# Optimization experiments

Hardware: AMD Instinct MI355X
Metric: run time of the kernel (lower is better)

## Reference

```python
import jax, jax.numpy as jnp
import numpy as np

N_NODES = 10000
N_EDGES = 640000
D_IN = 128
D_OUT = 128


def setup_inputs() -> dict:
    key = jax.random.key(0)
    k_x, k_val, k_w, k_row, k_col = jax.random.split(key, 5)
    # Glorot init for weight, zeros for bias (matches _weight_init)
    limit = float(np.sqrt(6.0 / (D_IN + D_OUT)))
    weight = jax.random.uniform(k_w, (D_IN, D_OUT), jnp.float32, -limit, limit)
    return {
        "x": jax.random.normal(k_x, (N_NODES, D_IN), jnp.float32),
        "adj_val": jax.random.uniform(k_val, (N_EDGES,), jnp.float32),  # normalized edge weights of sparse adj
        "weight": weight,
        "bias": jnp.zeros((D_OUT,), jnp.float32),
        "adj_row": jax.random.randint(k_row, (N_EDGES,), 0, N_NODES, jnp.int32),
        "adj_col": jax.random.randint(k_col, (N_EDGES,), 0, N_NODES, jnp.int32),
    }


def reference(x, adj_val, weight, bias, adj_row, adj_col):
    # dense GEMM: h = x @ W  -> [N, D_OUT]
    h = jnp.matmul(x, weight)
    # SpMM with COO adjacency: out[r] = sum_{e: row[e]=r} val[e] * h[col[e]]
    msg = adj_val[:, None] * h[adj_col]  # [E, D_OUT] gather + scale
    out = jax.ops.segment_sum(msg, adj_row, num_segments=x.shape[0])
    return out + bias
```

## Files before the change

kernel.cpp:

```cpp
#include <hip/hip_runtime.h>

#define N_NODES 10000
#define N_EDGES 640000
#define D 128
#define NQ (N_EDGES / 4)

#define NCHUNK 128
#define QPC (NQ / NCHUNK)
#define GEMM_BLOCKS 157
#define GRID1 (NCHUNK + GEMM_BLOCKS)
#define NBUCK 625
#define CCAP 24
#define BSLOTS (NCHUNK * CCAP)
#define SPILLCAP 5000
#define CAP2 128
#define QPAD2 144
#define LSTR 136

typedef unsigned int uint32;
typedef unsigned short u16;
using short8 = __attribute__((ext_vector_type(8))) short;
using f32x4  = __attribute__((ext_vector_type(4))) float;

__device__ __forceinline__ uint32 f2bf_bits(float f) {
    uint32 u = __float_as_uint(f);
    return (u + 0x7FFFu + ((u >> 16) & 1u)) >> 16;
}
__device__ __forceinline__ uint32 pack2(float lo, float hi) {
    return f2bf_bits(lo) | (f2bf_bits(hi) << 16);
}

__global__ __launch_bounds__(256, 4) void gemm_scatter_kernel(
    const float* __restrict__ x, const float* __restrict__ w,
    const int* __restrict__ row, const int* __restrict__ col,
    const float* __restrict__ val,
    uint32* __restrict__ h2, int* __restrict__ cnts,
    int* __restrict__ spillcnt, uint2* __restrict__ bstore,
    uint2* __restrict__ spill)
{
    __shared__ __align__(16) u16 Ws[128 * LSTR];
    const int t = threadIdx.x;

    if (blockIdx.x < NCHUNK) {
        int* lcnt = (int*)Ws;
        for (int i = t; i <= NBUCK; i += 256) lcnt[i] = 0;
        __syncthreads();

        const int sb = blockIdx.x;
        const int4*   row4 = (const int4*)row;
        const int4*   col4 = (const int4*)col;
        const float4* val4 = (const float4*)val;
        const int i0 = sb * QPC;
        for (int i = i0 + t; i < i0 + QPC; i += 256) {
            int4 r = row4[i]; int4 c = col4[i]; float4 v = val4[i];
            #pragma unroll
            for (int e = 0; e < 4; ++e) {
                int rr = (e == 0) ? r.x : (e == 1) ? r.y : (e == 2) ? r.z : r.w;
                int cc = (e == 0) ? c.x : (e == 1) ? c.y : (e == 2) ? c.z : c.w;
                float vv = (e == 0) ? v.x : (e == 1) ? v.y : (e == 2) ? v.z : v.w;
                uint32 rc = (uint32)cc | (f2bf_bits(vv) << 16);
                int b = rr >> 4;
                int k = atomicAdd(&lcnt[b], 1);
                if (k < CCAP)
                    bstore[(size_t)(b * NCHUNK + sb) * CCAP + k] =
                        make_uint2(rc, (uint32)rr);
                else {
                    int ks = atomicAdd(&lcnt[NBUCK], 1);
                    spill[(size_t)sb * SPILLCAP + ks] = make_uint2(rc, (uint32)rr);
                }
            }
        }
        __syncthreads();
        for (int b = t; b < NBUCK; b += 256) {
            int c = lcnt[b];
            cnts[b * NCHUNK + sb] = (c < CCAP) ? c : CCAP;
        }
        if (t == 0) spillcnt[sb] = lcnt[NBUCK];
    } else {
        const int g = blockIdx.x - NCHUNK;
        const int lane = t & 63;
        const int wid  = t >> 6;
        const int q = lane >> 4, cl = lane & 15;

        const float4* w4 = (const float4*)w;
        #pragma unroll
        for (int i = 0; i < 8; ++i) {
            int lin = t + i * 256;
            int m  = lin >> 5;
            int qc = lin & 31;
            float4 r0 = w4[(2 * m) * 32 + qc];
            float4 r1 = w4[(2 * m + 1) * 32 + qc];
            int c = qc * 4;
            *(uint32*)&Ws[(c + 0) * LSTR + 2 * m] = pack2(r0.x, r1.x);
            *(uint32*)&Ws[(c + 1) * LSTR + 2 * m] = pack2(r0.y, r1.y);
            *(uint32*)&Ws[(c + 2) * LSTR + 2 * m] = pack2(r0.z, r1.z);
            *(uint32*)&Ws[(c + 3) * LSTR + 2 * m] = pack2(r0.w, r1.w);
        }

        int gr = g * 64 + wid * 16 + cl;
        if (gr >= N_NODES) gr = N_NODES - 1;
        const float* xrow = &x[(size_t)gr * D];
        float4 xv[8];
        #pragma unroll
        for (int kk = 0; kk < 4; ++kk) {
            xv[2 * kk]     = *(const float4*)&xrow[kk * 32 + q * 8];
            xv[2 * kk + 1] = *(const float4*)&xrow[kk * 32 + q * 8 + 4];
        }
        __syncthreads();

        f32x4 acc[8] = {};
        #pragma unroll
        for (int kk = 0; kk < 4; ++kk) {
            union { short8 s; uint32 u[4]; } af;
            float4 a = xv[2 * kk], b = xv[2 * kk + 1];
            af.u[0] = pack2(a.x, a.y); af.u[1] = pack2(a.z, a.w);
            af.u[2] = pack2(b.x, b.y); af.u[3] = pack2(b.z, b.w);
            #pragma unroll
            for (int ct = 0; ct < 8; ++ct) {
                short8 bf = *(const short8*)&Ws[(ct * 16 + cl) * LSTR + kk * 32 + q * 8];
                acc[ct] = __builtin_amdgcn_mfma_f32_16x16x32_bf16(af.s, bf, acc[ct], 0, 0, 0);
            }
        }
        #pragma unroll
        for (int reg = 0; reg < 4; ++reg) {
            int node = g * 64 + wid * 16 + q * 4 + reg;
            if (node < N_NODES) {
                uint32* base = h2 + (size_t)node * 64 + cl;
                #pragma unroll
                for (int ct = 0; ct < 4; ++ct)
                    base[ct * 16] = pack2(acc[ct][reg], acc[ct + 4][reg]);
            }
        }
    }
}

__global__ __launch_bounds__(256) void spmm_kernel(
    const uint2* __restrict__ bstore, const int* __restrict__ cnts,
    const int* __restrict__ spillcnt, const uint2* __restrict__ spill,
    const uint32* __restrict__ h2, const float* __restrict__ bias,
    float* __restrict__ out)
{
    __shared__ uint32 qbuf[8 * QPAD2];
    __shared__ int lcnts[NCHUNK];
    __shared__ int cnt[8];
    const int t = threadIdx.x;
    const int lane = t & 63;
    const int wid  = t >> 6;
    const int r0 = blockIdx.x * 8;
    const int b  = r0 >> 4;

    if (t < NCHUNK) lcnts[t] = cnts[b * NCHUNK + t];
    if (t < 8) cnt[t] = 0;
    __syncthreads();

    const size_t sbase = (size_t)b * BSLOTS;
    for (int i = t; i < BSLOTS; i += 256) {
        int ch = i / CCAP;
        int sl = i - ch * CCAP;
        if (sl < lcnts[ch]) {
            uint2 e = bstore[sbase + i];
            uint32 d = e.y - (uint32)r0;
            if (d < 8u) {
                int k = atomicAdd(&cnt[d], 1);
                if (k < CAP2) qbuf[d * QPAD2 + k] = e.x;
            }
        }
    }
    if (t < NCHUNK) {
        int sc = spillcnt[t];
        for (int k = 0; k < sc; ++k) {
            uint2 e = spill[(size_t)t * SPILLCAP + k];
            uint32 d = e.y - (uint32)r0;
            if (d < 8u) {
                int k2 = atomicAdd(&cnt[d], 1);
                if (k2 < CAP2) qbuf[d * QPAD2 + k2] = e.x;
            }
        }
    }
    __syncthreads();

    for (int half = 0; half < 2; ++half) {
        const int d = wid * 2 + half;
        const int r = r0 + d;
        uint32* qb = &qbuf[d * QPAD2];
        const int ntot = cnt[d];
        float a0 = 0.f, a1 = 0.f;

        if (ntot <= CAP2) {
            if (lane < 16) qb[ntot + lane] = 0;
            __builtin_amdgcn_s_waitcnt(0);

            const int npad = (ntot + 7) & ~7;
            uint32 rq0,rq1,rq2,rq3,rq4,rq5,rq6,rq7;
            uint32 hh0,hh1,hh2,hh3,hh4,hh5,hh6,hh7;
            rq0 = qb[0]; hh0 = h2[((rq0 & 0xFFFFu) << 6) + lane];
            rq1 = qb[1]; hh1 = h2[((rq1 & 0xFFFFu) << 6) + lane];
            rq2 = qb[2]; hh2 = h2[((rq2 & 0xFFFFu) << 6) + lane];
            rq3 = qb[3]; hh3 = h2[((rq3 & 0xFFFFu) << 6) + lane];
            rq4 = qb[4]; hh4 = h2[((rq4 & 0xFFFFu) << 6) + lane];
            rq5 = qb[5]; hh5 = h2[((rq5 & 0xFFFFu) << 6) + lane];
            rq6 = qb[6]; hh6 = h2[((rq6 & 0xFFFFu) << 6) + lane];
            rq7 = qb[7]; hh7 = h2[((rq7 & 0xFFFFu) << 6) + lane];

#define CONSUME_PREFETCH(RQ, HH, P)                                          \
    {                                                                        \
        a0 = fmaf(__uint_as_float(RQ & 0xFFFF0000u),                         \
                  __uint_as_float(HH << 16), a0);                            \
        a1 = fmaf(__uint_as_float(RQ & 0xFFFF0000u),                         \
                  __uint_as_float(HH & 0xFFFF0000u), a1);                    \
        uint32 rn = qb[j + 8 + P];                                           \
        RQ = rn; HH = h2[((rn & 0xFFFFu) << 6) + lane];                      \
    }

            for (int j = 0; j < npad; j += 8) {
                CONSUME_PREFETCH(rq0, hh0, 0)
                CONSUME_PREFETCH(rq1, hh1, 1)
                CONSUME_PREFETCH(rq2, hh2, 2)
                CONSUME_PREFETCH(rq3, hh3, 3)
                CONSUME_PREFETCH(rq4, hh4, 4)
                CONSUME_PREFETCH(rq5, hh5, 5)
                CONSUME_PREFETCH(rq6, hh6, 6)
                CONSUME_PREFETCH(rq7, hh7, 7)
            }
#undef CONSUME_PREFETCH
        } else {
            for (int i = 0; i < BSLOTS; ++i) {
                int ch = i / CCAP, sl = i - ch * CCAP;
                if (sl < lcnts[ch]) {
                    uint2 e = bstore[sbase + i];
                    if (e.y == (uint32)r) {
                        uint32 hv = h2[((e.x & 0xFFFFu) << 6) + lane];
                        a0 = fmaf(__uint_as_float(e.x & 0xFFFF0000u),
                                  __uint_as_float(hv << 16), a0);
                        a1 = fmaf(__uint_as_float(e.x & 0xFFFF0000u),
                                  __uint_as_float(hv & 0xFFFF0000u), a1);
                    }
                }
            }
            for (int ch = 0; ch < NCHUNK; ++ch) {
                int sc = spillcnt[ch];
                for (int k = 0; k < sc; ++k) {
                    uint2 e = spill[(size_t)ch * SPILLCAP + k];
                    if (e.y == (uint32)r) {
                        uint32 hv = h2[((e.x & 0xFFFFu) << 6) + lane];
                        a0 = fmaf(__uint_as_float(e.x & 0xFFFF0000u),
                                  __uint_as_float(hv << 16), a0);
                        a1 = fmaf(__uint_as_float(e.x & 0xFFFF0000u),
                                  __uint_as_float(hv & 0xFFFF0000u), a1);
                    }
                }
            }
        }

        out[(size_t)r * D + lane]      = a0 + bias[lane];
        out[(size_t)r * D + 64 + lane] = a1 + bias[lane + 64];
    }
}

extern "C" void kernel_launch(void* const* d_in, const int* in_sizes, int n_in,
                              void* d_out, int out_size, void* d_ws, size_t ws_size,
                              hipStream_t stream)
{
    const float* x    = (const float*)d_in[0];
    const float* aval = (const float*)d_in[1];
    const float* w    = (const float*)d_in[2];
    const float* bias = (const float*)d_in[3];
    const int* arow   = (const int*)d_in[4];
    const int* acol   = (const int*)d_in[5];

    char* ws = (char*)d_ws;
    uint32* h2       = (uint32*)(ws);
    int*    cnts     = (int*)(ws + 2560000);
    int*    spillcnt = (int*)(ws + 2880000);
    uint2*  bstore   = (uint2*)(ws + 2880512);
    uint2*  spill    = (uint2*)(ws + 18240512);

    gemm_scatter_kernel<<<GRID1, 256, 0, stream>>>(
        x, w, arow, acol, aval, h2, cnts, spillcnt, bstore, spill);
    spmm_kernel<<<N_NODES / 8, 256, 0, stream>>>(
        bstore, cnts, spillcnt, spill, h2, bias, (float*)d_out);
}
```

Before: 103.7 us.

## Shrink buckets to 8 rows and compact per-wave queues with ballot instead of LDS atomics

Buckets now hold 8 destination rows instead of 16, so each SpMM block reads only its own bucket and discards no records, with per-chunk capacity cut to 16. Each wave now scans the whole bucket itself and builds its two row queues using ballot and popcount prefix sums rather than shared-memory atomics, which removes a block barrier. The spill scan is skipped when no chunk spilled. In exchange every wave reads all bucket slots redundantly, and the smaller capacity makes spills more likely.

```diff
diff --git a/kernel.cpp b/kernel.cpp
--- a/kernel.cpp
+++ b/kernel.cpp
@@ -9,8 +9,8 @@
 #define QPC (NQ / NCHUNK)
 #define GEMM_BLOCKS 157
 #define GRID1 (NCHUNK + GEMM_BLOCKS)
-#define NBUCK 625
-#define CCAP 24
+#define NBUCK 1250
+#define CCAP 16
 #define BSLOTS (NCHUNK * CCAP)
 #define SPILLCAP 5000
 #define CAP2 128
@@ -18,6 +18,7 @@
 #define LSTR 136
 
 typedef unsigned int uint32;
+typedef unsigned long long u64;
 typedef unsigned short u16;
 using short8 = __attribute__((ext_vector_type(8))) short;
 using f32x4  = __attribute__((ext_vector_type(4))) float;
@@ -59,10 +60,10 @@
                 int cc = (e == 0) ? c.x : (e == 1) ? c.y : (e == 2) ? c.z : c.w;
                 float vv = (e == 0) ? v.x : (e == 1) ? v.y : (e == 2) ? v.z : v.w;
                 uint32 rc = (uint32)cc | (f2bf_bits(vv) << 16);
-                int b = rr >> 4;
+                int b = rr >> 3;
                 int k = atomicAdd(&lcnt[b], 1);
                 if (k < CCAP)
-                    bstore[(size_t)(b * NCHUNK + sb) * CCAP + k] =
+                    bstore[((size_t)(b * NCHUNK + sb) << 4) + k] =
                         make_uint2(rc, (uint32)rr);
                 else {
                     int ks = atomicAdd(&lcnt[NBUCK], 1);
@@ -142,65 +143,73 @@
 {
     __shared__ uint32 qbuf[8 * QPAD2];
     __shared__ int lcnts[NCHUNK];
-    __shared__ int cnt[8];
+    __shared__ int sany;
     const int t = threadIdx.x;
     const int lane = t & 63;
     const int wid  = t >> 6;
-    const int r0 = blockIdx.x * 8;
-    const int b  = r0 >> 4;
-
-    if (t < NCHUNK) lcnts[t] = cnts[b * NCHUNK + t];
-    if (t < 8) cnt[t] = 0;
+    const int b  = blockIdx.x;
+    const int r0 = b * 8;
+
+    if (t == 0) sany = 0;
     __syncthreads();
+    if (t < NCHUNK) {
+        lcnts[t] = cnts[b * NCHUNK + t];
+        if (spillcnt[t] != 0) atomicAdd(&sany, 1);
+    }
+    __syncthreads();
 
     const size_t sbase = (size_t)b * BSLOTS;
-    for (int i = t; i < BSLOTS; i += 256) {
-        int ch = i / CCAP;
-        int sl = i - ch * CCAP;
+    const uint32 da = (uint32)(wid * 2), db = da + 1;
+    uint32* qa = &qbuf[(wid * 2) * QPAD2];
+    uint32* qz = &qbuf[(wid * 2 + 1) * QPAD2];
+    int ca = 0, cb = 0;
+    const u64 pre = (lane == 63) ? ~0ull >> 1 : (1ull << lane) - 1;
+    #pragma unroll 4
+    for (int i = lane; i < BSLOTS; i += 64) {
+        int ch = i >> 4, sl = i & 15;
+        uint32 rec = 0, d = 0xFFFFFFFFu;
         if (sl < lcnts[ch]) {
             uint2 e = bstore[sbase + i];
-            uint32 d = e.y - (uint32)r0;
-            if (d < 8u) {
-                int k = atomicAdd(&cnt[d], 1);
-                if (k < CAP2) qbuf[d * QPAD2 + k] = e.x;
-            }
-        }
-    }
-    if (t < NCHUNK) {
-        int sc = spillcnt[t];
-        for (int k = 0; k < sc; ++k) {
-            uint2 e = spill[(size_t)t * SPILLCAP + k];
-            uint32 d = e.y - (uint32)r0;
-            if (d < 8u) {
-                int k2 = atomicAdd(&cnt[d], 1);
-                if (k2 < CAP2) qbuf[d * QPAD2 + k2] = e.x;
-            }
-        }
-    }
-    __syncthreads();
+            rec = e.x; d = e.y - (uint32)r0;
+        }
+        u64 ma = __ballot(d == da);
+        u64 mb = __ballot(d == db);
+        if (d == da) { int p = ca + __popcll(ma & pre); if (p < CAP2) qa[p] = rec; }
+        if (d == db) { int p = cb + __popcll(mb & pre); if (p < CAP2) qz[p] = rec; }
+        ca += __popcll(ma); cb += __popcll(mb);
+    }
+    if (sany) {
+        for (int ch = 0; ch < NCHUNK; ++ch) {
+            int sc = spillcnt[ch];
+            for (int k = 0; k < sc; ++k) {
+                uint2 e = spill[(size_t)ch * SPILLCAP + k];
+                if (e.y == (uint32)r0 + da) { if (lane == 0 && ca < CAP2) qa[ca] = e.x; ca++; }
+                if (e.y == (uint32)r0 + db) { if (lane == 0 && cb < CAP2) qz[cb] = e.x; cb++; }
+            }
+        }
+    }
 
     for (int half = 0; half < 2; ++half) {
-        const int d = wid * 2 + half;
-        const int r = r0 + d;
-        uint32* qb = &qbuf[d * QPAD2];
-        const int ntot = cnt[d];
+        const int r = r0 + wid * 2 + half;
+        uint32* qp = (half == 0) ? qa : qz;
+        const int ntot = (half == 0) ? ca : cb;
         float a0 = 0.f, a1 = 0.f;
 
         if (ntot <= CAP2) {
-            if (lane < 16) qb[ntot + lane] = 0;
+            if (lane < 16) qp[ntot + lane] = 0;
             __builtin_amdgcn_s_waitcnt(0);
 
             const int npad = (ntot + 7) & ~7;
             uint32 rq0,rq1,rq2,rq3,rq4,rq5,rq6,rq7;
             uint32 hh0,hh1,hh2,hh3,hh4,hh5,hh6,hh7;
-            rq0 = qb[0]; hh0 = h2[((rq0 & 0xFFFFu) << 6) + lane];
-            rq1 = qb[1]; hh1 = h2[((rq1 & 0xFFFFu) << 6) + lane];
-            rq2 = qb[2]; hh2 = h2[((rq2 & 0xFFFFu) << 6) + lane];
-            rq3 = qb[3]; hh3 = h2[((rq3 & 0xFFFFu) << 6) + lane];
-            rq4 = qb[4]; hh4 = h2[((rq4 & 0xFFFFu) << 6) + lane];
-            rq5 = qb[5]; hh5 = h2[((rq5 & 0xFFFFu) << 6) + lane];
-            rq6 = qb[6]; hh6 = h2[((rq6 & 0xFFFFu) << 6) + lane];
-            rq7 = qb[7]; hh7 = h2[((rq7 & 0xFFFFu) << 6) + lane];
+            rq0 = qp[0]; hh0 = h2[((rq0 & 0xFFFFu) << 6) + lane];
+            rq1 = qp[1]; hh1 = h2[((rq1 & 0xFFFFu) << 6) + lane];
+            rq2 = qp[2]; hh2 = h2[((rq2 & 0xFFFFu) << 6) + lane];
+            rq3 = qp[3]; hh3 = h2[((rq3 & 0xFFFFu) << 6) + lane];
+            rq4 = qp[4]; hh4 = h2[((rq4 & 0xFFFFu) << 6) + lane];
+            rq5 = qp[5]; hh5 = h2[((rq5 & 0xFFFFu) << 6) + lane];
+            rq6 = qp[6]; hh6 = h2[((rq6 & 0xFFFFu) << 6) + lane];
+            rq7 = qp[7]; hh7 = h2[((rq7 & 0xFFFFu) << 6) + lane];
 
 #define CONSUME_PREFETCH(RQ, HH, P)                                          \
     {                                                                        \
@@ -208,7 +217,7 @@
                   __uint_as_float(HH << 16), a0);                            \
         a1 = fmaf(__uint_as_float(RQ & 0xFFFF0000u),                         \
                   __uint_as_float(HH & 0xFFFF0000u), a1);                    \
-        uint32 rn = qb[j + 8 + P];                                           \
+        uint32 rn = qp[j + 8 + P];                                           \
         RQ = rn; HH = h2[((rn & 0xFFFFu) << 6) + lane];                      \
     }
 
@@ -225,7 +234,7 @@
 #undef CONSUME_PREFETCH
         } else {
             for (int i = 0; i < BSLOTS; ++i) {
-                int ch = i / CCAP, sl = i - ch * CCAP;
+                int ch = i >> 4, sl = i & 15;
                 if (sl < lcnts[ch]) {
                     uint2 e = bstore[sbase + i];
                     if (e.y == (uint32)r) {
@@ -271,12 +280,12 @@
     char* ws = (char*)d_ws;
     uint32* h2       = (uint32*)(ws);
     int*    cnts     = (int*)(ws + 2560000);
-    int*    spillcnt = (int*)(ws + 2880000);
-    uint2*  bstore   = (uint2*)(ws + 2880512);
-    uint2*  spill    = (uint2*)(ws + 18240512);
+    int*    spillcnt = (int*)(ws + 3200000);
+    uint2*  bstore   = (uint2*)(ws + 3200512);
+    uint2*  spill    = (uint2*)(ws + 23680512);
 
     gemm_scatter_kernel<<<GRID1, 256, 0, stream>>>(
         x, w, arow, acol, aval, h2, cnts, spillcnt, bstore, spill);
-    spmm_kernel<<<N_NODES / 8, 256, 0, stream>>>(
+    spmm_kernel<<<NBUCK, 256, 0, stream>>>(
         bstore, cnts, spillcnt, spill, h2, bias, (float*)d_out);
 }
```

Measured after the change: 111.2 us. +7.3%, slower.

## Fuse GEMM and COO scatter into warp-specialized 1024-thread blocks

Applied to the files above, without the earlier changes.

Merges the GEMM and edge-bucketing work into the same 1024-thread blocks. Four waves compute a 40-row slice of h via MFMA while the other twelve waves scatter edges into buckets. The chunk count rises from 128 to 250 and the per-chunk bucket capacity drops to 16, so the SpMM slot index uses shifts instead of division. The aim is to overlap the two kinds of work inside each CU and spread the scatter over more blocks. The cost is that each SpMM block now scans more bucket slots and reads a larger bucket store. The 1024-thread launch bounds may also constrain registers, and the divergent branches rely on matching barrier counts.

```diff
diff --git a/kernel.cpp b/kernel.cpp
--- a/kernel.cpp
+++ b/kernel.cpp
@@ -5,14 +5,13 @@
 #define D 128
 #define NQ (N_EDGES / 4)
 
-#define NCHUNK 128
+#define NCHUNK 250
 #define QPC (NQ / NCHUNK)
-#define GEMM_BLOCKS 157
-#define GRID1 (NCHUNK + GEMM_BLOCKS)
+#define ROWS_PB 40
 #define NBUCK 625
-#define CCAP 24
+#define CCAP 16
 #define BSLOTS (NCHUNK * CCAP)
-#define SPILLCAP 5000
+#define SPILLCAP 2560
 #define CAP2 128
 #define QPAD2 144
 #define LSTR 136
@@ -30,7 +29,7 @@
     return f2bf_bits(lo) | (f2bf_bits(hi) << 16);
 }
 
-__global__ __launch_bounds__(256, 4) void gemm_scatter_kernel(
+__global__ __launch_bounds__(1024, 4) void gemm_scatter_kernel(
     const float* __restrict__ x, const float* __restrict__ w,
     const int* __restrict__ row, const int* __restrict__ col,
     const float* __restrict__ val,
@@ -39,19 +38,20 @@
     uint2* __restrict__ spill)
 {
     __shared__ __align__(16) u16 Ws[128 * LSTR];
+    __shared__ int lcnt[NBUCK + 1];
     const int t = threadIdx.x;
-
-    if (blockIdx.x < NCHUNK) {
-        int* lcnt = (int*)Ws;
-        for (int i = t; i <= NBUCK; i += 256) lcnt[i] = 0;
-        __syncthreads();
-
-        const int sb = blockIdx.x;
+    const int sb = blockIdx.x;
+
+    if (t >= 256) {
+        const int st = t - 256;
+        for (int i = st; i <= NBUCK; i += 768) lcnt[i] = 0;
+        __syncthreads();
+
         const int4*   row4 = (const int4*)row;
         const int4*   col4 = (const int4*)col;
         const float4* val4 = (const float4*)val;
         const int i0 = sb * QPC;
-        for (int i = i0 + t; i < i0 + QPC; i += 256) {
+        for (int i = i0 + st; i < i0 + QPC; i += 768) {
             int4 r = row4[i]; int4 c = col4[i]; float4 v = val4[i];
             #pragma unroll
             for (int e = 0; e < 4; ++e) {
@@ -71,13 +71,12 @@
             }
         }
         __syncthreads();
-        for (int b = t; b < NBUCK; b += 256) {
+        for (int b = st; b < NBUCK; b += 768) {
             int c = lcnt[b];
             cnts[b * NCHUNK + sb] = (c < CCAP) ? c : CCAP;
         }
-        if (t == 0) spillcnt[sb] = lcnt[NBUCK];
+        if (st == 0) spillcnt[sb] = lcnt[NBUCK];
     } else {
-        const int g = blockIdx.x - NCHUNK;
         const int lane = t & 63;
         const int wid  = t >> 6;
         const int q = lane >> 4, cl = lane & 15;
@@ -96,41 +95,45 @@
             *(uint32*)&Ws[(c + 2) * LSTR + 2 * m] = pack2(r0.z, r1.z);
             *(uint32*)&Ws[(c + 3) * LSTR + 2 * m] = pack2(r0.w, r1.w);
         }
-
-        int gr = g * 64 + wid * 16 + cl;
-        if (gr >= N_NODES) gr = N_NODES - 1;
-        const float* xrow = &x[(size_t)gr * D];
-        float4 xv[8];
-        #pragma unroll
-        for (int kk = 0; kk < 4; ++kk) {
-            xv[2 * kk]     = *(const float4*)&xrow[kk * 32 + q * 8];
-            xv[2 * kk + 1] = *(const float4*)&xrow[kk * 32 + q * 8 + 4];
-        }
-        __syncthreads();
-
-        f32x4 acc[8] = {};
-        #pragma unroll
-        for (int kk = 0; kk < 4; ++kk) {
-            union { short8 s; uint32 u[4]; } af;
-            float4 a = xv[2 * kk], b = xv[2 * kk + 1];
-            af.u[0] = pack2(a.x, a.y); af.u[1] = pack2(a.z, a.w);
-            af.u[2] = pack2(b.x, b.y); af.u[3] = pack2(b.z, b.w);
-            #pragma unroll
-            for (int ct = 0; ct < 8; ++ct) {
-                short8 bf = *(const short8*)&Ws[(ct * 16 + cl) * LSTR + kk * 32 + q * 8];
-                acc[ct] = __builtin_amdgcn_mfma_f32_16x16x32_bf16(af.s, bf, acc[ct], 0, 0, 0);
-            }
-        }
-        #pragma unroll
-        for (int reg = 0; reg < 4; ++reg) {
-            int node = g * 64 + wid * 16 + q * 4 + reg;
-            if (node < N_NODES) {
-                uint32* base = h2 + (size_t)node * 64 + cl;
+        __syncthreads();
+
+        const int base = sb * ROWS_PB;
+        const int rend = base + ROWS_PB;
+        if (wid * 16 < ROWS_PB) {
+            int gr = base + wid * 16 + cl;
+            if (gr >= N_NODES) gr = N_NODES - 1;
+            const float* xrow = &x[(size_t)gr * D];
+            float4 xv[8];
+            #pragma unroll
+            for (int kk = 0; kk < 4; ++kk) {
+                xv[2 * kk]     = *(const float4*)&xrow[kk * 32 + q * 8];
+                xv[2 * kk + 1] = *(const float4*)&xrow[kk * 32 + q * 8 + 4];
+            }
+            f32x4 acc[8] = {};
+            #pragma unroll
+            for (int kk = 0; kk < 4; ++kk) {
+                union { short8 s; uint32 u[4]; } af;
+                float4 a = xv[2 * kk], b = xv[2 * kk + 1];
+                af.u[0] = pack2(a.x, a.y); af.u[1] = pack2(a.z, a.w);
+                af.u[2] = pack2(b.x, b.y); af.u[3] = pack2(b.z, b.w);
                 #pragma unroll
-                for (int ct = 0; ct < 4; ++ct)
-                    base[ct * 16] = pack2(acc[ct][reg], acc[ct + 4][reg]);
-            }
-        }
+                for (int ct = 0; ct < 8; ++ct) {
+                    short8 bf = *(const short8*)&Ws[(ct * 16 + cl) * LSTR + kk * 32 + q * 8];
+                    acc[ct] = __builtin_amdgcn_mfma_f32_16x16x32_bf16(af.s, bf, acc[ct], 0, 0, 0);
+                }
+            }
+            #pragma unroll
+            for (int reg = 0; reg < 4; ++reg) {
+                int node = base + wid * 16 + q * 4 + reg;
+                if (node < rend) {
+                    uint32* outp = h2 + (size_t)node * 64 + cl;
+                    #pragma unroll
+                    for (int ct = 0; ct < 4; ++ct)
+                        outp[ct * 16] = pack2(acc[ct][reg], acc[ct + 4][reg]);
+                }
+            }
+        }
+        __syncthreads();
     }
 }
 
@@ -155,8 +158,8 @@
 
     const size_t sbase = (size_t)b * BSLOTS;
     for (int i = t; i < BSLOTS; i += 256) {
-        int ch = i / CCAP;
-        int sl = i - ch * CCAP;
+        int ch = i >> 4;
+        int sl = i & 15;
         if (sl < lcnts[ch]) {
             uint2 e = bstore[sbase + i];
             uint32 d = e.y - (uint32)r0;
@@ -225,7 +228,7 @@
 #undef CONSUME_PREFETCH
         } else {
             for (int i = 0; i < BSLOTS; ++i) {
-                int ch = i / CCAP, sl = i - ch * CCAP;
+                int ch = i >> 4, sl = i & 15;
                 if (sl < lcnts[ch]) {
                     uint2 e = bstore[sbase + i];
                     if (e.y == (uint32)r) {
@@ -271,11 +274,11 @@
     char* ws = (char*)d_ws;
     uint32* h2       = (uint32*)(ws);
     int*    cnts     = (int*)(ws + 2560000);
-    int*    spillcnt = (int*)(ws + 2880000);
-    uint2*  bstore   = (uint2*)(ws + 2880512);
-    uint2*  spill    = (uint2*)(ws + 18240512);
-
-    gemm_scatter_kernel<<<GRID1, 256, 0, stream>>>(
+    int*    spillcnt = (int*)(ws + 3185000);
+    uint2*  bstore   = (uint2*)(ws + 3186048);
+    uint2*  spill    = (uint2*)(ws + 23186048);
+
+    gemm_scatter_kernel<<<NCHUNK, 1024, 0, stream>>>(
         x, w, arow, acol, aval, h2, cnts, spillcnt, bstore, spill);
     spmm_kernel<<<N_NODES / 8, 256, 0, stream>>>(
         bstore, cnts, spillcnt, spill, h2, bias, (float*)d_out);
```

Result: no change. 104.1 us (+0.5%).
